# Performance work log

Measured on AMD Instinct MI355X. Metric: run time of the kernel, lower is better.

The kernel has to match this reference:

```python
import jax, jax.numpy as jnp
import numpy as np

B, H, S, DK, DV = 2, 8, 2048, 64, 64


def _alibi_bias(num_heads, q_len, k_len, dtype=jnp.float32):
    # standard ALiBi slopes: 2^(-8h/H) for h = 1..H
    slopes = 2.0 ** (-8.0 * jnp.arange(1, num_heads + 1, dtype=dtype) / num_heads)
    # relative distance bias: -(i - j), zero on/above diagonal matters only pre-mask
    dist = jnp.arange(k_len, dtype=dtype)[None, :] - jnp.arange(q_len, dtype=dtype)[:, None]
    return (slopes[:, None, None] * dist[None, :, :])[None]  # (1, H, S, S)


def setup_inputs() -> dict:
    key = jax.random.key(0)
    kq, kk, kv = jax.random.split(key, 3)
    query = jax.random.normal(kq, (B, H, S, DK), dtype=jnp.float32)
    key_t = jax.random.normal(kk, (B, H, S, DK), dtype=jnp.float32)
    value = jax.random.normal(kv, (B, H, S, DV), dtype=jnp.float32)
    # causal mask: positions with 1 are masked (j > i)
    mask = jnp.triu(jnp.ones((S, S), dtype=jnp.int32), k=1)[None, None]  # (1,1,S,S)
    alibi_bias = _alibi_bias(H, S, S)  # (1,H,S,S)
    return {"query": query, "key": key_t, "value": value, "mask": mask, "alibi_bias": alibi_bias}


def reference(query, key, value, mask, alibi_bias):
    d_k = query.shape[-1]
    scale = 1.0 / jnp.sqrt(jnp.asarray(d_k, dtype=jnp.float32))
    # scores: (B, H, S, S)
    scores = jnp.einsum("bhqd,bhkd->bhqk", query, key) * scale
    scores = scores + alibi_bias
    scores = jnp.where(mask == 1, -jnp.inf, scores)
    attention_weights = jax.nn.softmax(scores, axis=-1)
    output = jnp.einsum("bhqk,bhkd->bhqd", attention_weights, value)
    return output, attention_weights
```

## Files before the change

### kernel.cpp

```cpp
#include <hip/hip_runtime.h>
#include <math.h>

#define BB 2
#define HH 8
#define SS 2048
#define DD 64
#define NBH (BB*HH)

typedef float f32x4 __attribute__((ext_vector_type(4)));
typedef short bf16x8 __attribute__((ext_vector_type(8)));
typedef short bf16x4 __attribute__((ext_vector_type(4)));

static __device__ __forceinline__ short f2bf(float x) {
    unsigned u = __float_as_uint(x);
    u = (u + 0x7fffu + ((u >> 16) & 1u)) >> 16;
    return (short)u;
}

__global__ __launch_bounds__(256) void prep_qk(const float* __restrict__ Q,
                                               const float* __restrict__ K,
                                               short* __restrict__ Qb,
                                               short* __restrict__ Kb)
{
    const int n4 = NBH * SS * DD / 4;
    for (int idx = blockIdx.x * 256 + threadIdx.x; idx < n4; idx += gridDim.x * 256) {
        float4 q = ((const float4*)Q)[idx];
        float4 k = ((const float4*)K)[idx];
        bf16x4 qo, ko;
        qo[0] = f2bf(0.125f * q.x); qo[1] = f2bf(0.125f * q.y);
        qo[2] = f2bf(0.125f * q.z); qo[3] = f2bf(0.125f * q.w);
        ko[0] = f2bf(k.x); ko[1] = f2bf(k.y); ko[2] = f2bf(k.z); ko[3] = f2bf(k.w);
        ((bf16x4*)Qb)[idx] = qo;
        ((bf16x4*)Kb)[idx] = ko;
    }
}

__global__ __launch_bounds__(256) void prep_vt(const float* __restrict__ V,
                                               short* __restrict__ Vt)
{
    __shared__ short t[64][72];
    const int jt = blockIdx.x, bh = blockIdx.y;
    const int tid = threadIdx.x;
    const int r  = tid >> 2;
    const int c4 = (tid & 3) * 16;
    const float* vb = V + ((size_t)bh * SS + (size_t)jt * 64) * DD;
    #pragma unroll
    for (int cc = 0; cc < 4; ++cc) {
        float4 v = *(const float4*)(vb + r * DD + c4 + cc * 4);
        t[c4 + cc*4 + 0][r] = f2bf(v.x);
        t[c4 + cc*4 + 1][r] = f2bf(v.y);
        t[c4 + cc*4 + 2][r] = f2bf(v.z);
        t[c4 + cc*4 + 3][r] = f2bf(v.w);
    }
    __syncthreads();
    short* ob = Vt + ((size_t)bh * DD + r) * SS + (size_t)jt * 64 + c4;
    *(bf16x8*)ob       = *(bf16x8*)&t[r][c4];
    *(bf16x8*)(ob + 8) = *(bf16x8*)&t[r][c4 + 8];
}

__global__ __launch_bounds__(512, 4) void attn_main(
    const short* __restrict__ Qb, const short* __restrict__ Kb,
    const short* __restrict__ Vt,
    float* __restrict__ out, float* __restrict__ wts)
{
    const int flat = blockIdx.x;
    const int wg   = (flat & 7) * 64 + (flat >> 3);
    const int bh   = wg >> 5;
    const int pr   = wg & 31;
    const int h    = bh & 7;

    const int tid  = threadIdx.x;
    const int wv   = tid >> 6;
    const int lane = tid & 63;
    const int g    = lane >> 4;
    const int c16  = lane & 15;

    __shared__ float smo[8][16][65];
    __shared__ float lred[8][2][16];

    const short* Kp = Kb + (size_t)bh * SS * DD;
    const short* Vp = Vt + (size_t)bh * DD * SS;

    const float slope = exp2f(-(float)(h + 1));

    int kk8[8]; float offc[8];
    #pragma unroll
    for (int t = 0; t < 2; ++t)
        #pragma unroll
        for (int r = 0; r < 4; ++r) {
            kk8[t*4+r]  = 16*t + 4*g + r;
            offc[t*4+r] = slope * (float)(16*t + 4*g + r);
        }

    #pragma unroll 1
    for (int it = 0; it < 2; ++it) {
        const int qt     = (it == 0) ? pr : 63 - pr;
        const int q0     = qt * 32;
        const int nsteps = qt + 1;
        const int cover  = q0 + 32;

        const short* Qp = Qb + ((size_t)bh * SS + q0) * DD;
        float* wbase = wts + ((size_t)bh * SS + q0) * (size_t)SS;
        float* obase = out + ((size_t)bh * SS + q0) * DD;

        {
            const int n4 = (SS - cover) >> 2;
            const f32x4 z = {0.f, 0.f, 0.f, 0.f};
            for (int r = 0; r < 32; ++r) {
                float* wr = wbase + (size_t)r * SS + cover;
                for (int c = tid; c < n4; c += 512) ((f32x4*)wr)[c] = z;
            }
        }

        bf16x8 qf[2][2];
        #pragma unroll
        for (int qh = 0; qh < 2; ++qh)
            #pragma unroll
            for (int c = 0; c < 2; ++c)
                qf[qh][c] = *(const bf16x8*)(Qp + (size_t)(qh*16 + c16) * DD + c*32 + g*8);

        float l[2] = {0.f, 0.f};
        for (int s = wv; s < nsteps; s += 8) {
            const int j0 = s * 32;
            bf16x8 kf[2][2];
            #pragma unroll
            for (int t = 0; t < 2; ++t)
                #pragma unroll
                for (int c = 0; c < 2; ++c)
                    kf[t][c] = *(const bf16x8*)(Kp + (size_t)(j0 + 16*t + c16) * DD + c*32 + g*8);

            f32x4 acc[2][2];
            #pragma unroll
            for (int qh = 0; qh < 2; ++qh)
                #pragma unroll
                for (int t = 0; t < 2; ++t)
                    acc[qh][t] = (f32x4){0.f, 0.f, 0.f, 0.f};
            #pragma unroll
            for (int qh = 0; qh < 2; ++qh)
                #pragma unroll
                for (int t = 0; t < 2; ++t)
                    #pragma unroll
                    for (int c = 0; c < 2; ++c)
                        acc[qh][t] = __builtin_amdgcn_mfma_f32_16x16x32_bf16(kf[t][c], qf[qh][c], acc[qh][t], 0, 0, 0);

            const bool diag = (s == qt);
            #pragma unroll
            for (int qh = 0; qh < 2; ++qh) {
                const int   irow = q0 + qh*16 + c16;
                const float sb   = slope * (float)(j0 - irow);
                const int   lim  = irow - j0;
                float ls = 0.f;
                #pragma unroll
                for (int u = 0; u < 8; ++u) {
                    float e = __expf(acc[qh][u>>2][u&3] + sb + offc[u]);
                    if (diag) e = (kk8[u] <= lim) ? e : 0.f;
                    ls += e;
                }
                l[qh] += ls;
            }
        }
        #pragma unroll
        for (int qh = 0; qh < 2; ++qh) {
            l[qh] += __shfl_xor(l[qh], 16, 64);
            l[qh] += __shfl_xor(l[qh], 32, 64);
        }

        if (lane < 16) {
            #pragma unroll
            for (int qh = 0; qh < 2; ++qh) lred[wv][qh][lane] = l[qh];
        }
        __syncthreads();
        float invl[2];
        #pragma unroll
        for (int qh = 0; qh < 2; ++qh) {
            float lf = 0.f;
            #pragma unroll
            for (int w2 = 0; w2 < 8; ++w2) lf += lred[w2][qh][c16];
            invl[qh] = 1.f / lf;
        }

        f32x4 oacc[2][4];
        #pragma unroll
        for (int qh = 0; qh < 2; ++qh)
            #pragma unroll
            for (int d0 = 0; d0 < 4; ++d0) oacc[qh][d0] = (f32x4){0.f, 0.f, 0.f, 0.f};

        for (int s = wv; s < nsteps; s += 8) {
            const int j0 = s * 32;
            bf16x8 kf[2][2];
            #pragma unroll
            for (int t = 0; t < 2; ++t)
                #pragma unroll
                for (int c = 0; c < 2; ++c)
                    kf[t][c] = *(const bf16x8*)(Kp + (size_t)(j0 + 16*t + c16) * DD + c*32 + g*8);

            f32x4 acc[2][2];
            #pragma unroll
            for (int qh = 0; qh < 2; ++qh)
                #pragma unroll
                for (int t = 0; t < 2; ++t)
                    acc[qh][t] = (f32x4){0.f, 0.f, 0.f, 0.f};
            #pragma unroll
            for (int qh = 0; qh < 2; ++qh)
                #pragma unroll
                for (int t = 0; t < 2; ++t)
                    #pragma unroll
                    for (int c = 0; c < 2; ++c)
                        acc[qh][t] = __builtin_amdgcn_mfma_f32_16x16x32_bf16(kf[t][c], qf[qh][c], acc[qh][t], 0, 0, 0);

            const bool diag = (s == qt);
            bf16x8 wf[2];
            #pragma unroll
            for (int qh = 0; qh < 2; ++qh) {
                const int   irow = q0 + qh*16 + c16;
                const float sb   = slope * (float)(j0 - irow);
                const int   lim  = irow - j0;
                float w8[8];
                #pragma unroll
                for (int u = 0; u < 8; ++u) {
                    float e = __expf(acc[qh][u>>2][u&3] + sb + offc[u]);
                    if (diag) e = (kk8[u] <= lim) ? e : 0.f;
                    w8[u] = e * invl[qh];
                }
                float* wr0 = wbase + (size_t)(qh*16 + c16) * SS + j0 + 4*g;
                *(f32x4*)wr0        = (f32x4){w8[0], w8[1], w8[2], w8[3]};
                *(f32x4*)(wr0 + 16) = (f32x4){w8[4], w8[5], w8[6], w8[7]};
                #pragma unroll
                for (int u = 0; u < 8; ++u) wf[qh][u] = f2bf(w8[u]);
            }

            const short* vp = Vp + j0;
            #pragma unroll
            for (int d0 = 0; d0 < 4; ++d0) {
                const short* vr = vp + (size_t)(d0*16 + c16) * SS;
                bf16x4 a  = *(const bf16x4*)(vr + 4*g);
                bf16x4 b2 = *(const bf16x4*)(vr + 16 + 4*g);
                bf16x8 vf;
                vf[0]=a[0]; vf[1]=a[1]; vf[2]=a[2]; vf[3]=a[3];
                vf[4]=b2[0]; vf[5]=b2[1]; vf[6]=b2[2]; vf[7]=b2[3];
                #pragma unroll
                for (int qh = 0; qh < 2; ++qh)
                    oacc[qh][d0] = __builtin_amdgcn_mfma_f32_16x16x32_bf16(vf, wf[qh], oacc[qh][d0], 0, 0, 0);
            }
        }

        __syncthreads();
        #pragma unroll
        for (int qh = 0; qh < 2; ++qh) {
            #pragma unroll
            for (int d0 = 0; d0 < 4; ++d0)
                *(f32x4*)&smo[wv][c16][d0*16 + 4*g] = oacc[qh][d0];
            __syncthreads();
            if (tid < 256) {
                int q = tid >> 4, dc = tid & 15;
                f32x4 r = {0.f, 0.f, 0.f, 0.f};
                #pragma unroll
                for (int w2 = 0; w2 < 8; ++w2) r += *(f32x4*)&smo[w2][q][dc * 4];
                *(f32x4*)(obase + (size_t)(qh*16 + q) * DD + dc * 4) = r;
            }
            __syncthreads();
        }
    }
}

extern "C" void kernel_launch(void* const* d_in, const int* in_sizes, int n_in,
                              void* d_out, int out_size, void* d_ws, size_t ws_size,
                              hipStream_t stream) {
    const float* Q = (const float*)d_in[0];
    const float* K = (const float*)d_in[1];
    const float* V = (const float*)d_in[2];

    float* out = (float*)d_out;
    float* wts = out + (size_t)BB * HH * SS * DD;

    const size_t n = (size_t)NBH * SS * DD;
    short* Qb = (short*)d_ws;
    short* Kb = Qb + n;
    short* Vt = Kb + n;

    prep_qk<<<dim3(1024), dim3(256), 0, stream>>>(Q, K, Qb, Kb);
    prep_vt<<<dim3(SS / 64, NBH), dim3(256), 0, stream>>>(V, Vt);

    attn_main<<<dim3(512), dim3(512), 0, stream>>>(Qb, Kb, Vt, out, wts);
}
```

Before: 106.6 us.

## Merge prep kernels and double-buffer K fragment loads in attention loops

```diff
diff --git a/kernel.cpp b/kernel.cpp
--- a/kernel.cpp
+++ b/kernel.cpp
@@ -17,45 +17,45 @@
     return (short)u;
 }
 
-__global__ __launch_bounds__(256) void prep_qk(const float* __restrict__ Q,
-                                               const float* __restrict__ K,
-                                               short* __restrict__ Qb,
-                                               short* __restrict__ Kb)
-{
-    const int n4 = NBH * SS * DD / 4;
-    for (int idx = blockIdx.x * 256 + threadIdx.x; idx < n4; idx += gridDim.x * 256) {
-        float4 q = ((const float4*)Q)[idx];
-        float4 k = ((const float4*)K)[idx];
-        bf16x4 qo, ko;
-        qo[0] = f2bf(0.125f * q.x); qo[1] = f2bf(0.125f * q.y);
-        qo[2] = f2bf(0.125f * q.z); qo[3] = f2bf(0.125f * q.w);
-        ko[0] = f2bf(k.x); ko[1] = f2bf(k.y); ko[2] = f2bf(k.z); ko[3] = f2bf(k.w);
-        ((bf16x4*)Qb)[idx] = qo;
-        ((bf16x4*)Kb)[idx] = ko;
-    }
-}
-
-__global__ __launch_bounds__(256) void prep_vt(const float* __restrict__ V,
-                                               short* __restrict__ Vt)
+__global__ __launch_bounds__(256) void prep_all(const float* __restrict__ Q,
+                                                const float* __restrict__ K,
+                                                const float* __restrict__ V,
+                                                short* __restrict__ Qb,
+                                                short* __restrict__ Kb,
+                                                short* __restrict__ Vt)
 {
     __shared__ short t[64][72];
-    const int jt = blockIdx.x, bh = blockIdx.y;
     const int tid = threadIdx.x;
-    const int r  = tid >> 2;
-    const int c4 = (tid & 3) * 16;
-    const float* vb = V + ((size_t)bh * SS + (size_t)jt * 64) * DD;
-    #pragma unroll
-    for (int cc = 0; cc < 4; ++cc) {
-        float4 v = *(const float4*)(vb + r * DD + c4 + cc * 4);
-        t[c4 + cc*4 + 0][r] = f2bf(v.x);
-        t[c4 + cc*4 + 1][r] = f2bf(v.y);
-        t[c4 + cc*4 + 2][r] = f2bf(v.z);
-        t[c4 + cc*4 + 3][r] = f2bf(v.w);
+    if (blockIdx.x < 512) {
+        const int jt = blockIdx.x & 31, bh = blockIdx.x >> 5;
+        const int r  = tid >> 2;
+        const int c4 = (tid & 3) * 16;
+        const float* vb = V + ((size_t)bh * SS + (size_t)jt * 64) * DD;
+        #pragma unroll
+        for (int cc = 0; cc < 4; ++cc) {
+            float4 v = *(const float4*)(vb + r * DD + c4 + cc * 4);
+            t[c4 + cc*4 + 0][r] = f2bf(v.x);
+            t[c4 + cc*4 + 1][r] = f2bf(v.y);
+            t[c4 + cc*4 + 2][r] = f2bf(v.z);
+            t[c4 + cc*4 + 3][r] = f2bf(v.w);
+        }
+        __syncthreads();
+        short* ob = Vt + ((size_t)bh * DD + r) * SS + (size_t)jt * 64 + c4;
+        *(bf16x8*)ob       = *(bf16x8*)&t[r][c4];
+        *(bf16x8*)(ob + 8) = *(bf16x8*)&t[r][c4 + 8];
+    } else {
+        const int n4 = NBH * SS * DD / 4;
+        for (int idx = (blockIdx.x - 512) * 256 + tid; idx < n4; idx += 1024 * 256) {
+            float4 q = ((const float4*)Q)[idx];
+            float4 k = ((const float4*)K)[idx];
+            bf16x4 qo, ko;
+            qo[0] = f2bf(0.125f * q.x); qo[1] = f2bf(0.125f * q.y);
+            qo[2] = f2bf(0.125f * q.z); qo[3] = f2bf(0.125f * q.w);
+            ko[0] = f2bf(k.x); ko[1] = f2bf(k.y); ko[2] = f2bf(k.z); ko[3] = f2bf(k.w);
+            ((bf16x4*)Qb)[idx] = qo;
+            ((bf16x4*)Kb)[idx] = ko;
+        }
     }
-    __syncthreads();
-    short* ob = Vt + ((size_t)bh * DD + r) * SS + (size_t)jt * 64 + c4;
-    *(bf16x8*)ob       = *(bf16x8*)&t[r][c4];
-    *(bf16x8*)(ob + 8) = *(bf16x8*)&t[r][c4 + 8];
 }
 
 __global__ __launch_bounds__(512, 4) void attn_main(
@@ -119,44 +119,59 @@
             for (int c = 0; c < 2; ++c)
                 qf[qh][c] = *(const bf16x8*)(Qp + (size_t)(qh*16 + c16) * DD + c*32 + g*8);
 
-        float l[2] = {0.f, 0.f};
-        for (int s = wv; s < nsteps; s += 8) {
+        const int n_it = (nsteps > wv) ? ((nsteps - wv + 7) >> 3) : 0;
+        const int n2   = (n_it + 1) & ~1;
+
+        auto loadK = [&](bf16x8 (&kf)[2][2], int s) {
             const int j0 = s * 32;
-            bf16x8 kf[2][2];
             #pragma unroll
             for (int t = 0; t < 2; ++t)
                 #pragma unroll
                 for (int c = 0; c < 2; ++c)
                     kf[t][c] = *(const bf16x8*)(Kp + (size_t)(j0 + 16*t + c16) * DD + c*32 + g*8);
-
-            f32x4 acc[2][2];
-            #pragma unroll
-            for (int qh = 0; qh < 2; ++qh)
-                #pragma unroll
-                for (int t = 0; t < 2; ++t)
-                    acc[qh][t] = (f32x4){0.f, 0.f, 0.f, 0.f};
-            #pragma unroll
-            for (int qh = 0; qh < 2; ++qh)
-                #pragma unroll
-                for (int t = 0; t < 2; ++t)
-                    #pragma unroll
-                    for (int c = 0; c < 2; ++c)
-                        acc[qh][t] = __builtin_amdgcn_mfma_f32_16x16x32_bf16(kf[t][c], qf[qh][c], acc[qh][t], 0, 0, 0);
-
-            const bool diag = (s == qt);
-            #pragma unroll
-            for (int qh = 0; qh < 2; ++qh) {
-                const int   irow = q0 + qh*16 + c16;
-                const float sb   = slope * (float)(j0 - irow);
-                const int   lim  = irow - j0;
-                float ls = 0.f;
-                #pragma unroll
-                for (int u = 0; u < 8; ++u) {
-                    float e = __expf(acc[qh][u>>2][u&3] + sb + offc[u]);
-                    if (diag) e = (kk8[u] <= lim) ? e : 0.f;
-                    ls += e;
+        };
+
+        float l[2] = {0.f, 0.f};
+        if (n2 > 0) {
+            auto accum = [&](bf16x8 (&kf)[2][2], int s) {
+                f32x4 acc[2][2];
+                #pragma unroll
+                for (int qh = 0; qh < 2; ++qh)
+                    #pragma unroll
+                    for (int t = 0; t < 2; ++t)
+                        acc[qh][t] = (f32x4){0.f, 0.f, 0.f, 0.f};
+                #pragma unroll
+                for (int qh = 0; qh < 2; ++qh)
+                    #pragma unroll
+                    for (int t = 0; t < 2; ++t)
+                        #pragma unroll
+                        for (int c = 0; c < 2; ++c)
+                            acc[qh][t] = __builtin_amdgcn_mfma_f32_16x16x32_bf16(kf[t][c], qf[qh][c], acc[qh][t], 0, 0, 0);
+                const int j0 = s * 32;
+                #pragma unroll
+                for (int qh = 0; qh < 2; ++qh) {
+                    const int   irow = q0 + qh*16 + c16;
+                    const float sb   = slope * (float)(j0 - irow);
+                    const int   lim  = irow - j0;
+                    float ls = 0.f;
+                    #pragma unroll
+                    for (int u = 0; u < 8; ++u) {
+                        float e = __expf(acc[qh][u>>2][u&3] + sb + offc[u]);
+                        e = (kk8[u] <= lim) ? e : 0.f;
+                        ls += e;
+                    }
+                    l[qh] += ls;
                 }
-                l[qh] += ls;
+            };
+            bf16x8 kA[2][2], kB[2][2];
+            loadK(kA, wv);
+            int sA = wv;
+            #pragma unroll 1
+            for (int i = 0; i < n2; i += 2, sA += 16) {
+                loadK(kB, sA + 8);
+                accum(kA, sA);
+                if (i + 2 < n2) loadK(kA, sA + 16);
+                accum(kB, sA + 8);
             }
         }
         #pragma unroll
@@ -185,62 +200,67 @@
             #pragma unroll
             for (int d0 = 0; d0 < 4; ++d0) oacc[qh][d0] = (f32x4){0.f, 0.f, 0.f, 0.f};
 
-        for (int s = wv; s < nsteps; s += 8) {
-            const int j0 = s * 32;
-            bf16x8 kf[2][2];
-            #pragma unroll
-            for (int t = 0; t < 2; ++t)
-                #pragma unroll
-                for (int c = 0; c < 2; ++c)
-                    kf[t][c] = *(const bf16x8*)(Kp + (size_t)(j0 + 16*t + c16) * DD + c*32 + g*8);
-
-            f32x4 acc[2][2];
-            #pragma unroll
-            for (int qh = 0; qh < 2; ++qh)
-                #pragma unroll
-                for (int t = 0; t < 2; ++t)
-                    acc[qh][t] = (f32x4){0.f, 0.f, 0.f, 0.f};
-            #pragma unroll
-            for (int qh = 0; qh < 2; ++qh)
-                #pragma unroll
-                for (int t = 0; t < 2; ++t)
-                    #pragma unroll
-                    for (int c = 0; c < 2; ++c)
-                        acc[qh][t] = __builtin_amdgcn_mfma_f32_16x16x32_bf16(kf[t][c], qf[qh][c], acc[qh][t], 0, 0, 0);
-
-            const bool diag = (s == qt);
-            bf16x8 wf[2];
-            #pragma unroll
-            for (int qh = 0; qh < 2; ++qh) {
-                const int   irow = q0 + qh*16 + c16;
-                const float sb   = slope * (float)(j0 - irow);
-                const int   lim  = irow - j0;
-                float w8[8];
-                #pragma unroll
-                for (int u = 0; u < 8; ++u) {
-                    float e = __expf(acc[qh][u>>2][u&3] + sb + offc[u]);
-                    if (diag) e = (kk8[u] <= lim) ? e : 0.f;
-                    w8[u] = e * invl[qh];
+        if (n2 > 0) {
+            auto proc = [&](bf16x8 (&kf)[2][2], int s) {
+                f32x4 acc[2][2];
+                #pragma unroll
+                for (int qh = 0; qh < 2; ++qh)
+                    #pragma unroll
+                    for (int t = 0; t < 2; ++t)
+                        acc[qh][t] = (f32x4){0.f, 0.f, 0.f, 0.f};
+                #pragma unroll
+                for (int qh = 0; qh < 2; ++qh)
+                    #pragma unroll
+                    for (int t = 0; t < 2; ++t)
+                        #pragma unroll
+                        for (int c = 0; c < 2; ++c)
+                            acc[qh][t] = __builtin_amdgcn_mfma_f32_16x16x32_bf16(kf[t][c], qf[qh][c], acc[qh][t], 0, 0, 0);
+                const int  j0   = s * 32;
+                const bool live = (s < nsteps);
+                bf16x8 wf[2];
+                #pragma unroll
+                for (int qh = 0; qh < 2; ++qh) {
+                    const int   irow = q0 + qh*16 + c16;
+                    const float sb   = slope * (float)(j0 - irow);
+                    const int   lim  = irow - j0;
+                    float w8[8];
+                    #pragma unroll
+                    for (int u = 0; u < 8; ++u) {
+                        float e = __expf(acc[qh][u>>2][u&3] + sb + offc[u]);
+                        e = (kk8[u] <= lim) ? e : 0.f;
+                        w8[u] = e * invl[qh];
+                    }
+                    if (live) {
+                        float* wr0 = wbase + (size_t)(qh*16 + c16) * SS + j0 + 4*g;
+                        *(f32x4*)wr0        = (f32x4){w8[0], w8[1], w8[2], w8[3]};
+                        *(f32x4*)(wr0 + 16) = (f32x4){w8[4], w8[5], w8[6], w8[7]};
+                    }
+                    #pragma unroll
+                    for (int u = 0; u < 8; ++u) wf[qh][u] = f2bf(w8[u]);
                 }
-                float* wr0 = wbase + (size_t)(qh*16 + c16) * SS + j0 + 4*g;
-                *(f32x4*)wr0        = (f32x4){w8[0], w8[1], w8[2], w8[3]};
-                *(f32x4*)(wr0 + 16) = (f32x4){w8[4], w8[5], w8[6], w8[7]};
-                #pragma unroll
-                for (int u = 0; u < 8; ++u) wf[qh][u] = f2bf(w8[u]);
-            }
-
-            const short* vp = Vp + j0;
-            #pragma unroll
-            for (int d0 = 0; d0 < 4; ++d0) {
-                const short* vr = vp + (size_t)(d0*16 + c16) * SS;
-                bf16x4 a  = *(const bf16x4*)(vr + 4*g);
-                bf16x4 b2 = *(const bf16x4*)(vr + 16 + 4*g);
-                bf16x8 vf;
-                vf[0]=a[0]; vf[1]=a[1]; vf[2]=a[2]; vf[3]=a[3];
-                vf[4]=b2[0]; vf[5]=b2[1]; vf[6]=b2[2]; vf[7]=b2[3];
-                #pragma unroll
-                for (int qh = 0; qh < 2; ++qh)
-                    oacc[qh][d0] = __builtin_amdgcn_mfma_f32_16x16x32_bf16(vf, wf[qh], oacc[qh][d0], 0, 0, 0);
+                const short* vp = Vp + j0;
+                #pragma unroll
+                for (int d0 = 0; d0 < 4; ++d0) {
+                    const short* vr = vp + (size_t)(d0*16 + c16) * SS;
+                    bf16x4 a  = *(const bf16x4*)(vr + 4*g);
+                    bf16x4 b2 = *(const bf16x4*)(vr + 16 + 4*g);
+                    bf16x8 vf;
+                    vf[0]=a[0]; vf[1]=a[1]; vf[2]=a[2]; vf[3]=a[3];
+                    vf[4]=b2[0]; vf[5]=b2[1]; vf[6]=b2[2]; vf[7]=b2[3];
+                    #pragma unroll
+                    for (int qh = 0; qh < 2; ++qh)
+                        oacc[qh][d0] = __builtin_amdgcn_mfma_f32_16x16x32_bf16(vf, wf[qh], oacc[qh][d0], 0, 0, 0);
+                }
+            };
+            bf16x8 kA[2][2], kB[2][2];
+            loadK(kA, wv);
+            int sA = wv;
+            #pragma unroll 1
+            for (int i = 0; i < n2; i += 2, sA += 16) {
+                loadK(kB, sA + 8);
+                proc(kA, sA);
+                if (i + 2 < n2) loadK(kA, sA + 16);
+                proc(kB, sA + 8);
             }
         }
 
@@ -278,8 +298,7 @@
     short* Kb = Qb + n;
     short* Vt = Kb + n;
 
-    prep_qk<<<dim3(1024), dim3(256), 0, stream>>>(Q, K, Qb, Kb);
-    prep_vt<<<dim3(SS / 64, NBH), dim3(256), 0, stream>>>(V, Vt);
+    prep_all<<<dim3(1536), dim3(256), 0, stream>>>(Q, K, V, Qb, Kb, Vt);
 
     attn_main<<<dim3(512), dim3(512), 0, stream>>>(Qb, Kb, Vt, out, wts);
 }
```

Result: slower. 168.1 us (+57.8%).
